# Kernel optimization log

Measured on AMD Instinct MI355X. Metric: run time of the kernel, lower is better.

The kernel has to match this reference:

```python
import jax, jax.numpy as jnp
import numpy as np

N, C, H, W = 8, 256, 64, 64
NW = 8            # n_win (regions per side)
TOPK = 4
HEADS = 16
MLP = 4 * C
SCALE = C ** -0.5  # qk_dim = dim in BiLevelRoutingAttention


def _ln(x, g, b, eps=1e-6):
    mu = x.mean(-1, keepdims=True)
    var = ((x - mu) ** 2).mean(-1, keepdims=True)
    return (x - mu) * jax.lax.rsqrt(var + eps) * g + b


def setup_inputs() -> dict:
    key = jax.random.key(0)
    ks = jax.random.split(key, 8)
    f = lambda k, shp: jax.random.normal(k, shp, jnp.float32) * 0.02
    return {
        "x": jax.random.normal(ks[0], (N, C, H, W), jnp.float32),
        "norm1_g": jnp.ones((C,), jnp.float32), "norm1_b": jnp.zeros((C,), jnp.float32),
        "qkv_w": f(ks[1], (C, 3 * C)), "qkv_b": jnp.zeros((3 * C,), jnp.float32),
        "lepe_w": f(ks[2], (5, 5, 1, C)), "lepe_b": jnp.zeros((C,), jnp.float32),
        "gamma1": -jnp.ones((C,), jnp.float32), "gamma2": -jnp.ones((C,), jnp.float32),
        "norm2_g": jnp.ones((C,), jnp.float32), "norm2_b": jnp.zeros((C,), jnp.float32),
        "mlp_w1": f(ks[3], (C, MLP)), "mlp_b1": jnp.zeros((MLP,), jnp.float32),
        "mlp_w2": f(ks[4], (MLP, C)), "mlp_b2": jnp.zeros((C,), jnp.float32),
    }


def _bra(x, qkv_w, qkv_b, lepe_w, lepe_b):
    # BiLevelRoutingAttention: x is NHWC
    n, hh, ww, c = x.shape
    h, w = hh // NW, ww // NW
    P, hw = NW * NW, h * w
    qkv = x @ qkv_w + qkv_b                    # [n,H,W,3c]
    q, k, v = qkv[..., :c], qkv[..., c:2 * c], qkv[..., 2 * c:]

    def win(t):                                 # [n,H,W,d] -> [n,P,h,w,d]
        d = t.shape[-1]
        return t.reshape(n, NW, h, NW, w, d).transpose(0, 1, 3, 2, 4, 5).reshape(n, P, h, w, d)

    qw, kw, vw = win(q), win(k), win(v)
    q_pix = qw.reshape(n, P, hw, c)
    k_pix = kw.reshape(n, P, hw, c)
    v_pix = vw.reshape(n, P, hw, c)

    # region-level routing (q/k detached; routing weights unused since mul_weight='none')
    q_win = jax.lax.stop_gradient(qw.mean((2, 3)))   # [n,P,c]
    k_win = jax.lax.stop_gradient(kw.mean((2, 3)))
    logit = jnp.einsum('npc,nqc->npq', q_win * SCALE, k_win)
    _, idx = jax.lax.top_k(logit, TOPK)              # [n,P,TOPK]

    gather = jax.vmap(lambda t, i: t[i])             # over batch
    k_sel = gather(k_pix, idx)                       # [n,P,TOPK,hw,c]
    v_sel = gather(v_pix, idx)

    dh = c // HEADS
    # channel layout is (m c): split heads on last dim
    qh = q_pix.reshape(n, P, hw, HEADS, dh).transpose(0, 1, 3, 2, 4)                       # [n,P,m,hw,dh]
    kh = k_sel.reshape(n, P, TOPK, hw, HEADS, dh).transpose(0, 1, 4, 2, 3, 5).reshape(n, P, HEADS, TOPK * hw, dh)
    vh = v_sel.reshape(n, P, TOPK, hw, HEADS, dh).transpose(0, 1, 4, 2, 3, 5).reshape(n, P, HEADS, TOPK * hw, dh)

    attn = jax.nn.softmax(jnp.einsum('npmqd,npmkd->npmqk', qh * SCALE, kh), axis=-1)
    out = jnp.einsum('npmqk,npmkd->npmqd', attn, vh)                                       # [n,P,m,hw,dh]
    out = out.transpose(0, 1, 3, 2, 4).reshape(n, P, hw, c)
    out = out.reshape(n, NW, NW, h, w, c).transpose(0, 1, 3, 2, 4, 5).reshape(n, hh, ww, c)

    # lepe: 5x5 depthwise conv over full-image v (side_dwconv=5)
    lepe = jax.lax.conv_general_dilated(
        v, lepe_w, (1, 1), 'SAME',
        dimension_numbers=('NHWC', 'HWIO', 'NHWC'),
        feature_group_count=c) + lepe_b
    return out + lepe   # wo = Identity for param_attention='qkv'


def reference(x, norm1_g, norm1_b, qkv_w, qkv_b, lepe_w, lepe_b, gamma1, gamma2,
              norm2_g, norm2_b, mlp_w1, mlp_b1, mlp_w2, mlp_b2):
    xp = x.transpose(0, 2, 3, 1)  # NCHW -> NHWC
    xp = xp + gamma1 * _bra(_ln(xp, norm1_g, norm1_b), qkv_w, qkv_b, lepe_w, lepe_b)
    z = _ln(xp, norm2_g, norm2_b)
    m = jax.nn.gelu(z @ mlp_w1 + mlp_b1, approximate=False) @ mlp_w2 + mlp_b2
    xp = xp + gamma2 * m
    return xp.transpose(0, 3, 1, 2)  # NHWC -> NCHW
```

## Files before the change

kernel.cpp:

```cpp
#include <hip/hip_runtime.h>

typedef unsigned short u16;
typedef __bf16 bf16x8 __attribute__((ext_vector_type(8)));
typedef short s16x4 __attribute__((ext_vector_type(4)));
typedef float f32x4 __attribute__((ext_vector_type(4)));

#define SCALE_ATT 0.0625f

static __device__ __forceinline__ u16 f2b(float f) {
    union { float f; unsigned u; } v; v.f = f;
    unsigned r = (v.u + 0x7fffu + ((v.u >> 16) & 1u)) >> 16;
    return (u16)r;
}
static __device__ __forceinline__ float b2f(u16 h) {
    union { unsigned u; float f; } v; v.u = ((unsigned)h) << 16;
    return v.f;
}

#if defined(__has_builtin)
#if __has_builtin(__builtin_amdgcn_mfma_f32_16x16x16bf16_1k)
#define HAVE_MFMA16 1
#endif
#if __has_builtin(__builtin_amdgcn_exp2f)
#define EXP2(x) __builtin_amdgcn_exp2f(x)
#endif
#if __has_builtin(__builtin_amdgcn_global_load_lds)
#define HAVE_GLOADLDS 1
#endif
#endif
#ifndef EXP2
#define EXP2(x) exp2f(x)
#endif

static __device__ __forceinline__ f32x4 mfma16(s16x4 a, s16x4 b, f32x4 c) {
#ifdef HAVE_MFMA16
    return __builtin_amdgcn_mfma_f32_16x16x16bf16_1k(a, b, c, 0, 0, 0);
#else
    f32x4 d;
    asm volatile("v_mfma_f32_16x16x16_bf16 %0, %1, %2, %3\n\ts_nop 7\n\ts_nop 7"
                 : "=v"(d) : "v"(a), "v"(b), "v"(c));
    return d;
#endif
}

#ifdef HAVE_GLOADLDS
static __device__ __forceinline__ void gload16(const u16* g, u16* l) {
    __builtin_amdgcn_global_load_lds(
        (const __attribute__((address_space(1))) void*)g,
        (__attribute__((address_space(3))) void*)l, 16, 0, 0);
}
#endif

__global__ void wtrans_kernel(const float* __restrict__ src, u16* __restrict__ dst,
                              int R, int C) {
    int i = blockIdx.x * 256 + threadIdx.x;
    if (i >= R * C) return;
    int r = i / C, c = i % C;
    dst[(size_t)c * R + r] = f2b(src[i]);
}

__global__ __launch_bounds__(256) void ln_xpose_kernel(
    const float* __restrict__ x, const float* __restrict__ g, const float* __restrict__ b,
    float* __restrict__ xp, u16* __restrict__ ln1, float* __restrict__ pool_part) {
    __shared__ float xs[256][65];
    __shared__ float ps[4][64], ps2[4][64];
    __shared__ float mvmu[64], mvrs[64];
    int nb = blockIdx.x; int n = nb >> 6, y = nb & 63;
    int t = threadIdx.x;
    const float4* src = (const float4*)(x + ((size_t)(n * 256 + t) * 64 + y) * 64);
    for (int x4 = 0; x4 < 16; ++x4) {
        float4 v = src[x4];
        xs[t][x4 * 4 + 0] = v.x; xs[t][x4 * 4 + 1] = v.y;
        xs[t][x4 * 4 + 2] = v.z; xs[t][x4 * 4 + 3] = v.w;
    }
    __syncthreads();
    int part = t >> 6, l = t & 63;
    float s1 = 0.f, s2 = 0.f;
    for (int c = 0; c < 64; ++c) { float v = xs[part * 64 + c][l]; s1 += v; s2 += v * v; }
    ps[part][l] = s1; ps2[part][l] = s2;
    __syncthreads();
    if (t < 64) {
        float su = ps[0][t] + ps[1][t] + ps[2][t] + ps[3][t];
        float sq = ps2[0][t] + ps2[1][t] + ps2[2][t] + ps2[3][t];
        float mu = su * (1.f / 256.f);
        float var = sq * (1.f / 256.f) - mu * mu;
        mvmu[t] = mu; mvrs[t] = rsqrtf(var + 1e-6f);
    }
    __syncthreads();
    float gc = g[t], bc = b[t];
    size_t tokbase = (size_t)nb * 64;
    float pw = 0.f;
    for (int xx = 0; xx < 64; ++xx) {
        float raw = xs[t][xx];
        float val = (raw - mvmu[xx]) * mvrs[xx] * gc + bc;
        size_t tok = tokbase + xx;
        xp[tok * 256 + t] = raw;
        ln1[tok * 256 + t] = f2b(val);
        pw += val;
        if ((xx & 7) == 7) {
            pool_part[((size_t)nb * 8 + (xx >> 3)) * 256 + t] = pw;
            pw = 0.f;
        }
    }
}

__global__ void pool_reduce_kernel(const float* __restrict__ pool_part,
                                   float* __restrict__ pooled) {
    int nb = blockIdx.x; int n = nb >> 6, p = nb & 63;
    int wi = p >> 3, wj = p & 7;
    int t = threadIdx.x;
    float s = 0.f;
    for (int r = 0; r < 8; ++r)
        s += pool_part[((size_t)((n * 64 + wi * 8 + r) * 8 + wj)) * 256 + t];
    pooled[(size_t)nb * 256 + t] = s * (1.f / 64.f);
}

__global__ void qkwin_kernel(const float* __restrict__ pooled,
                             const float* __restrict__ qkv_w, const float* __restrict__ qkv_b,
                             float* __restrict__ qk_win) {
    __shared__ float pr[256];
    int nb = blockIdx.x; int t = threadIdx.x;
    pr[t] = pooled[(size_t)nb * 256 + t];
    __syncthreads();
    float aq = qkv_b[t], ak = qkv_b[256 + t];
    for (int k = 0; k < 256; ++k) {
        float pv = pr[k];
        aq += pv * qkv_w[(size_t)k * 768 + t];
        ak += pv * qkv_w[(size_t)k * 768 + 256 + t];
    }
    qk_win[(size_t)nb * 512 + t] = aq;
    qk_win[(size_t)nb * 512 + 256 + t] = ak;
}

__global__ void routing_kernel(const float* __restrict__ qk_win, int* __restrict__ idxp) {
    __shared__ float lg_[64];
    int nb = blockIdx.x; int n = nb >> 6;
    int t = threadIdx.x;
    const float* qw = qk_win + (size_t)nb * 512;
    const float* kw = qk_win + (size_t)(n * 64 + t) * 512 + 256;
    float s = 0.f;
    for (int c = 0; c < 256; ++c) s += qw[c] * kw[c];
    lg_[t] = s * SCALE_ATT;
    __syncthreads();
    if (t == 0) {
        for (int j = 0; j < 4; ++j) {
            float best = -INFINITY; int bi = 0;
            for (int q = 0; q < 64; ++q) if (lg_[q] > best) { best = lg_[q]; bi = q; }
            idxp[nb * 4 + j] = bi;
            lg_[bi] = -INFINITY;
        }
    }
}

template <int EPI>
__global__ __launch_bounds__(256) void gemm_kernel(
    const u16* __restrict__ A, const u16* __restrict__ Bt,
    const float* __restrict__ bias, u16* __restrict__ outb,
    int M, int Nn, int K,
    const float* __restrict__ resid_in, const float* __restrict__ gamma,
    float* __restrict__ resid_out) {
    __shared__ u16 As[4096];
    __shared__ u16 Bs[4096];
    int t = threadIdx.x;
    int rowBase = blockIdx.x * 128, colBase = blockIdx.y * 128;
    int wid = t >> 6, lane = t & 63;
    int wr = (wid >> 1) * 64, wc = (wid & 1) * 64;
    int lr = lane & 15, g = lane >> 4;
    f32x4 acc[4][4] = {};

    int rA0 = wid * 32 + (lane >> 2);
    int rA1 = rA0 + 16;
    int cs0 = (lane & 3) ^ ((rA0 >> 1) & 3);
    int cs1 = (lane & 3) ^ ((rA1 >> 1) & 3);
    const u16* gA0 = A + (size_t)(rowBase + rA0) * K + cs0 * 8;
    const u16* gA1 = A + (size_t)(rowBase + rA1) * K + cs1 * 8;
    const u16* gB0 = Bt + (size_t)(colBase + rA0) * K + cs0 * 8;
    const u16* gB1 = Bt + (size_t)(colBase + rA1) * K + cs1 * 8;
    u16* lA0 = &As[(wid * 2 + 0) * 512];
    u16* lA1 = &As[(wid * 2 + 1) * 512];
    u16* lB0 = &Bs[(wid * 2 + 0) * 512];
    u16* lB1 = &Bs[(wid * 2 + 1) * 512];

    int cSwz = (g * 16) ^ (((lr >> 1) & 3) << 4);
    const char* pA = (const char*)As;
    const char* pB = (const char*)Bs;

    for (int k0 = 0; k0 < K; k0 += 32) {
#ifdef HAVE_GLOADLDS
        gload16(gA0 + k0, lA0);
        gload16(gA1 + k0, lA1);
        gload16(gB0 + k0, lB0);
        gload16(gB1 + k0, lB1);
        __syncthreads();
#else
        float4 a0 = *(const float4*)(gA0 + k0);
        float4 a1 = *(const float4*)(gA1 + k0);
        float4 b0 = *(const float4*)(gB0 + k0);
        float4 b1 = *(const float4*)(gB1 + k0);
        __syncthreads();
        *(float4*)&lA0[lane * 8] = a0;
        *(float4*)&lA1[lane * 8] = a1;
        *(float4*)&lB0[lane * 8] = b0;
        *(float4*)&lB1[lane * 8] = b1;
        __syncthreads();
#endif
        bf16x8 af[4], bfr[4];
        #pragma unroll
        for (int m = 0; m < 4; ++m)
            af[m] = *(const bf16x8*)(pA + (wr + m * 16 + lr) * 64 + cSwz);
        #pragma unroll
        for (int nn = 0; nn < 4; ++nn)
            bfr[nn] = *(const bf16x8*)(pB + (wc + nn * 16 + lr) * 64 + cSwz);
        #pragma unroll
        for (int m = 0; m < 4; ++m)
            #pragma unroll
            for (int nn = 0; nn < 4; ++nn)
                acc[m][nn] = __builtin_amdgcn_mfma_f32_16x16x32_bf16(af[m], bfr[nn], acc[m][nn], 0, 0, 0);
        __syncthreads();
    }
    #pragma unroll
    for (int m = 0; m < 4; ++m)
        #pragma unroll
        for (int nn = 0; nn < 4; ++nn) {
            int col = colBase + wc + nn * 16 + lr;
            float bcol = bias[col];
            #pragma unroll
            for (int r = 0; r < 4; ++r) {
                int row = rowBase + wr + m * 16 + g * 4 + r;
                float v = acc[m][nn][r] + bcol;
                if constexpr (EPI == 0) {
                    outb[(size_t)row * Nn + col] = f2b(v);
                } else if constexpr (EPI == 1) {
                    float gl = 0.5f * v * (1.f + erff(v * 0.70710678118654752f));
                    outb[(size_t)row * Nn + col] = f2b(gl);
                } else {
                    float yv = resid_in[(size_t)row * 256 + col] + gamma[col] * v;
                    resid_out[(size_t)row * 256 + col] = yv;
                }
            }
        }
}

__global__ __launch_bounds__(256) void lepe_kernel(
    const u16* __restrict__ qkv, const float* __restrict__ w,
    const float* __restrict__ bias, u16* __restrict__ lepe) {
    __shared__ u16 vt[5][64][64];
    int nb = blockIdx.x, cg = blockIdx.y;
    int n = nb >> 6, y = nb & 63;
    int t = threadIdx.x;
    {
        int xs = t >> 3, cs = t & 7;
        #pragma unroll
        for (int r = 0; r < 5; ++r) {
            int yy = y - 2 + r;
            bool ok = (yy >= 0 && yy <= 63);
            #pragma unroll
            for (int half = 0; half < 2; ++half) {
                int x = xs + half * 32;
                float4 v = {0.f, 0.f, 0.f, 0.f};
                if (ok)
                    v = *(const float4*)(qkv +
                        ((size_t)((n * 64 + yy) * 64 + x)) * 768 + 512 + cg * 64 + cs * 8);
                *(float4*)&vt[r][x][cs * 8] = v;
            }
        }
    }
    __syncthreads();
    int c = t & 63, x0 = (t >> 6) * 16;
    float wv[25];
    #pragma unroll
    for (int i = 0; i < 25; ++i) wv[i] = w[i * 256 + cg * 64 + c];
    float bc = bias[cg * 64 + c];
    float win[5][5];
    #pragma unroll
    for (int r = 0; r < 5; ++r)
        #pragma unroll
        for (int j = 0; j < 4; ++j) {
            int x2 = x0 - 2 + j;
            win[r][j] = (x2 >= 0) ? b2f(vt[r][x2][c]) : 0.f;
        }
    #pragma unroll
    for (int xi = 0; xi < 16; ++xi) {
        int xx = x0 + xi;
        int xl = xx + 2;
        #pragma unroll
        for (int r = 0; r < 5; ++r)
            win[r][4] = (xl <= 63) ? b2f(vt[r][xl][c]) : 0.f;
        float s = bc;
        #pragma unroll
        for (int r = 0; r < 5; ++r)
            #pragma unroll
            for (int j = 0; j < 5; ++j)
                s = fmaf(wv[r * 5 + j], win[r][j], s);
        lepe[((size_t)nb * 64 + xx) * 256 + cg * 64 + c] = f2b(s);
        #pragma unroll
        for (int r = 0; r < 5; ++r)
            #pragma unroll
            for (int j = 0; j < 4; ++j)
                win[r][j] = win[r][j + 1];
    }
}

__global__ __launch_bounds__(512) void attn_kernel(
    const u16* __restrict__ qkv, const int* __restrict__ idxp,
    float* __restrict__ attn_out) {
    __shared__ __align__(16) char smem_[39424];
    u16 (*qs)[36]   = (u16 (*)[36])smem_;
    u16 (*ks)[36]   = (u16 (*)[36])(smem_ + 4608);
    u16 (*vts)[256] = (u16 (*)[256])(smem_ + 23040);
    float (*os)[36] = (float (*)[36])(smem_ + 4608);
    int nb = blockIdx.x, hg = blockIdx.y;
    int n = nb >> 6, p = nb & 63;
    int y0 = (p >> 3) * 8, x0 = (p & 7) * 8;
    int t = threadIdx.x;
    int w0 = idxp[nb * 4 + 0], w1 = idxp[nb * 4 + 1];
    int w2 = idxp[nb * 4 + 2], w3 = idxp[nb * 4 + 3];
    {
        int tok = t >> 3, seg = t & 7;
        int tokg = (n * 64 + y0 + (tok >> 3)) * 64 + x0 + (tok & 7);
        *(uint2*)&qs[tok][seg * 4] =
            *(const uint2*)(qkv + (size_t)tokg * 768 + hg * 32 + seg * 4);
    }
    {
        int key = t & 255, half = t >> 8;
        int ws = (key >> 6) == 0 ? w0 : (key >> 6) == 1 ? w1 : (key >> 6) == 2 ? w2 : w3;
        int kp = key & 63;
        int tokk = (n * 64 + (ws >> 3) * 8 + (kp >> 3)) * 64 + (ws & 7) * 8 + (kp & 7);
        const u16* kbase = qkv + (size_t)tokk * 768 + 256 + hg * 32 + half * 16;
        *(uint2*)&ks[key][half * 16 + 0]  = *(const uint2*)(kbase + 0);
        *(uint2*)&ks[key][half * 16 + 4]  = *(const uint2*)(kbase + 4);
        *(uint2*)&ks[key][half * 16 + 8]  = *(const uint2*)(kbase + 8);
        *(uint2*)&ks[key][half * 16 + 12] = *(const uint2*)(kbase + 12);
        const u16* vbase = kbase + 256;
        union { float4 f[2]; u16 u[16]; } vu;
        vu.f[0] = *(const float4*)vbase;
        vu.f[1] = *(const float4*)(vbase + 8);
        #pragma unroll
        for (int c2 = 0; c2 < 16; ++c2)
            vts[half * 16 + c2][key ^ (c2 << 2)] = vu.u[c2];
    }
    __syncthreads();

    int wid = t >> 6, lane = t & 63, lr = lane & 15, g = lane >> 4;
    int hh = wid & 1, q0 = (wid >> 1) * 16, c0 = hh * 16;
    f32x4 zf4 = {0.f, 0.f, 0.f, 0.f};
    s16x4 qf = *(const s16x4*)&qs[q0 + lr][c0 + g * 4];
    f32x4 sacc[16];
    __builtin_amdgcn_s_setprio(1);
    #pragma unroll
    for (int kt = 0; kt < 16; ++kt) {
        s16x4 kf = *(const s16x4*)&ks[kt * 16 + lr][c0 + g * 4];
        sacc[kt] = mfma16(kf, qf, zf4);
    }
    __builtin_amdgcn_s_setprio(0);
    float mx = fmaxf(fmaxf(sacc[0][0], sacc[0][1]), fmaxf(sacc[0][2], sacc[0][3]));
    #pragma unroll
    for (int kt = 1; kt < 16; ++kt) {
        mx = fmaxf(mx, fmaxf(sacc[kt][0], sacc[kt][1]));
        mx = fmaxf(mx, fmaxf(sacc[kt][2], sacc[kt][3]));
    }
    mx = fmaxf(mx, __shfl_xor(mx, 16, 64));
    mx = fmaxf(mx, __shfl_xor(mx, 32, 64));
    const float k1 = 0.09016844005556021f;
    float negmk = -mx * k1;
    float dsum = 0.f;
    s16x4 pf[16];
    #pragma unroll
    for (int kt = 0; kt < 16; ++kt) {
        float e0 = EXP2(fmaf(sacc[kt][0], k1, negmk));
        float e1 = EXP2(fmaf(sacc[kt][1], k1, negmk));
        float e2 = EXP2(fmaf(sacc[kt][2], k1, negmk));
        float e3 = EXP2(fmaf(sacc[kt][3], k1, negmk));
        dsum += (e0 + e1) + (e2 + e3);
        union { unsigned u[2]; s16x4 s; } pk;
        asm("v_cvt_pk_bf16_f32 %0, %1, %2" : "=v"(pk.u[0]) : "v"(e0), "v"(e1));
        asm("v_cvt_pk_bf16_f32 %0, %1, %2" : "=v"(pk.u[1]) : "v"(e2), "v"(e3));
        pf[kt] = pk.s;
    }
    dsum += __shfl_xor(dsum, 16, 64);
    dsum += __shfl_xor(dsum, 32, 64);
    float rden = 1.f / dsum;
    __syncthreads();
    f32x4 o0 = zf4, o1 = zf4;
    __builtin_amdgcn_s_setprio(1);
    #pragma unroll
    for (int kt = 0; kt < 16; kt += 2) {
        s16x4 v0 = *(const s16x4*)&vts[c0 + lr][(kt * 16 + g * 4) ^ (lr << 2)];
        o0 = mfma16(v0, pf[kt], o0);
        s16x4 v1 = *(const s16x4*)&vts[c0 + lr][((kt + 1) * 16 + g * 4) ^ (lr << 2)];
        o1 = mfma16(v1, pf[kt + 1], o1);
    }
    __builtin_amdgcn_s_setprio(0);
    #pragma unroll
    for (int r = 0; r < 4; ++r)
        os[q0 + lr][c0 + g * 4 + r] = (o0[r] + o1[r]) * rden;
    __syncthreads();
    {
        int tok = t >> 3, cs = (t & 7) * 4;
        int tokg = (n * 64 + y0 + (tok >> 3)) * 64 + x0 + (tok & 7);
        *(float4*)(attn_out + (size_t)tokg * 256 + hg * 32 + cs) =
            *(const float4*)&os[tok][cs];
    }
}

__global__ __launch_bounds__(256) void resid1_ln2_kernel(
    const float* __restrict__ xp, const float* __restrict__ attn,
    const u16* __restrict__ lepe, const float* __restrict__ g1,
    const float* __restrict__ n2g, const float* __restrict__ n2b,
    float* __restrict__ xp1, u16* __restrict__ z) {
    __shared__ float w1s[4], w2s[4];
    size_t tok = blockIdx.x;
    int t = threadIdx.x;
    float x1 = xp[tok * 256 + t] + g1[t] * (attn[tok * 256 + t] + b2f(lepe[tok * 256 + t]));
    xp1[tok * 256 + t] = x1;
    float s1 = x1, s2 = x1 * x1;
    for (int off = 1; off < 64; off <<= 1) {
        s1 += __shfl_xor(s1, off, 64);
        s2 += __shfl_xor(s2, off, 64);
    }
    int wid = t >> 6;
    if ((t & 63) == 0) { w1s[wid] = s1; w2s[wid] = s2; }
    __syncthreads();
    s1 = w1s[0] + w1s[1] + w1s[2] + w1s[3];
    s2 = w2s[0] + w2s[1] + w2s[2] + w2s[3];
    float mu = s1 * (1.f / 256.f);
    float var = s2 * (1.f / 256.f) - mu * mu;
    float rs = rsqrtf(var + 1e-6f);
    z[tok * 256 + t] = f2b((x1 - mu) * rs * n2g[t] + n2b[t]);
}

__global__ __launch_bounds__(256) void out_xpose_kernel(
    const float* __restrict__ yout, float* __restrict__ outp) {
    __shared__ float ys[256][65];
    int nb = blockIdx.x; int n = nb >> 6, y = nb & 63;
    int t = threadIdx.x;
    for (int xx = 0; xx < 64; ++xx)
        ys[t][xx] = yout[((size_t)nb * 64 + xx) * 256 + t];
    __syncthreads();
    float4* dst = (float4*)(outp + ((size_t)(n * 256 + t) * 64 + y) * 64);
    for (int x4 = 0; x4 < 16; ++x4) {
        float4 v = { ys[t][x4 * 4 + 0], ys[t][x4 * 4 + 1],
                     ys[t][x4 * 4 + 2], ys[t][x4 * 4 + 3] };
        dst[x4] = v;
    }
}

extern "C" void kernel_launch(void* const* d_in, const int* in_sizes, int n_in,
                              void* d_out, int out_size, void* d_ws, size_t ws_size,
                              hipStream_t stream) {
    (void)in_sizes; (void)n_in; (void)out_size; (void)ws_size;
    const float* x      = (const float*)d_in[0];
    const float* n1g    = (const float*)d_in[1];
    const float* n1b    = (const float*)d_in[2];
    const float* qkv_w  = (const float*)d_in[3];
    const float* qkv_b  = (const float*)d_in[4];
    const float* lepe_w = (const float*)d_in[5];
    const float* lepe_b = (const float*)d_in[6];
    const float* g1     = (const float*)d_in[7];
    const float* g2     = (const float*)d_in[8];
    const float* n2g    = (const float*)d_in[9];
    const float* n2b    = (const float*)d_in[10];
    const float* w1     = (const float*)d_in[11];
    const float* b1     = (const float*)d_in[12];
    const float* w2     = (const float*)d_in[13];
    const float* b2     = (const float*)d_in[14];
    float* outp = (float*)d_out;
    char* ws = (char*)d_ws;

    float* xp        = (float*)(ws + 0);
    u16*   ln1       = (u16*)(ws + 33554432);
    u16*   qkv       = (u16*)(ws + 50331648);
    float* attn_out  = (float*)(ws + 100663296);
    u16*   lepe      = (u16*)(ws + 134217728);
    u16*   zbuf      = (u16*)(ws + 150994944);
    float* pool_part = (float*)(ws + 167772160);
    float* pooled    = (float*)(ws + 171966464);
    float* qk_win    = (float*)(ws + 172490752);
    int*   idxb      = (int*)(ws + 173539328);
    u16*   wt_qkv    = (u16*)(ws + 173547520);
    u16*   wt_m1     = (u16*)(ws + 173940736);
    u16*   wt_m2     = (u16*)(ws + 174465024);
    u16*   hbuf      = ln1;
    float* xp1       = outp;
    float* yout      = attn_out;

    wtrans_kernel<<<768, 256, 0, stream>>>(qkv_w, wt_qkv, 256, 768);
    wtrans_kernel<<<1024, 256, 0, stream>>>(w1, wt_m1, 256, 1024);
    wtrans_kernel<<<1024, 256, 0, stream>>>(w2, wt_m2, 1024, 256);

    ln_xpose_kernel<<<512, 256, 0, stream>>>(x, n1g, n1b, xp, ln1, pool_part);
    pool_reduce_kernel<<<512, 256, 0, stream>>>(pool_part, pooled);
    qkwin_kernel<<<512, 256, 0, stream>>>(pooled, qkv_w, qkv_b, qk_win);
    routing_kernel<<<512, 64, 0, stream>>>(qk_win, idxb);

    gemm_kernel<0><<<dim3(256, 6), 256, 0, stream>>>(
        ln1, wt_qkv, qkv_b, qkv, 32768, 768, 256, nullptr, nullptr, nullptr);

    lepe_kernel<<<dim3(512, 4), 256, 0, stream>>>(qkv, lepe_w, lepe_b, lepe);
    attn_kernel<<<dim3(512, 8), 512, 0, stream>>>(qkv, idxb, attn_out);

    resid1_ln2_kernel<<<32768, 256, 0, stream>>>(xp, attn_out, lepe, g1, n2g, n2b, xp1, zbuf);

    gemm_kernel<1><<<dim3(256, 8), 256, 0, stream>>>(
        zbuf, wt_m1, b1, hbuf, 32768, 1024, 256, nullptr, nullptr, nullptr);
    gemm_kernel<2><<<dim3(256, 2), 256, 0, stream>>>(
        hbuf, wt_m2, b2, nullptr, 32768, 256, 1024, xp1, g2, yout);

    out_xpose_kernel<<<512, 256, 0, stream>>>(yout, outp);
}
```

Measured before the change: 278.4 us.

## Use tanh-approx GELU, bf16 attention output, and native bf16 conversion

```diff
diff --git a/kernel.cpp b/kernel.cpp
--- a/kernel.cpp
+++ b/kernel.cpp
@@ -8,9 +8,9 @@
 #define SCALE_ATT 0.0625f
 
 static __device__ __forceinline__ u16 f2b(float f) {
-    union { float f; unsigned u; } v; v.f = f;
-    unsigned r = (v.u + 0x7fffu + ((v.u >> 16) & 1u)) >> 16;
-    return (u16)r;
+    __bf16 h = (__bf16)f;
+    union { __bf16 b; u16 u; } v; v.b = h;
+    return v.u;
 }
 static __device__ __forceinline__ float b2f(u16 h) {
     union { unsigned u; float f; } v; v.u = ((unsigned)h) << 16;
@@ -24,12 +24,18 @@
 #if __has_builtin(__builtin_amdgcn_exp2f)
 #define EXP2(x) __builtin_amdgcn_exp2f(x)
 #endif
+#if __has_builtin(__builtin_amdgcn_rcpf)
+#define RCP(x) __builtin_amdgcn_rcpf(x)
+#endif
 #if __has_builtin(__builtin_amdgcn_global_load_lds)
 #define HAVE_GLOADLDS 1
 #endif
 #endif
 #ifndef EXP2
 #define EXP2(x) exp2f(x)
+#endif
+#ifndef RCP
+#define RCP(x) (1.0f / (x))
 #endif
 
 static __device__ __forceinline__ f32x4 mfma16(s16x4 a, s16x4 b, f32x4 c) {
@@ -50,6 +56,15 @@
         (__attribute__((address_space(3))) void*)l, 16, 0, 0);
 }
 #endif
+
+static __device__ __forceinline__ float gelu_fast(float v) {
+    float v2 = v * v;
+    float w = fmaf(v2, 0.044715f, 1.0f);
+    float arg = v * w * 2.30211754f;
+    float e = EXP2(arg);
+    float r = RCP(e + 1.0f);
+    return fmaf(-v, r, v);
+}
 
 __global__ void wtrans_kernel(const float* __restrict__ src, u16* __restrict__ dst,
                               int R, int C) {
@@ -231,8 +246,7 @@
                 if constexpr (EPI == 0) {
                     outb[(size_t)row * Nn + col] = f2b(v);
                 } else if constexpr (EPI == 1) {
-                    float gl = 0.5f * v * (1.f + erff(v * 0.70710678118654752f));
-                    outb[(size_t)row * Nn + col] = f2b(gl);
+                    outb[(size_t)row * Nn + col] = f2b(gelu_fast(v));
                 } else {
                     float yv = resid_in[(size_t)row * 256 + col] + gamma[col] * v;
                     resid_out[(size_t)row * 256 + col] = yv;
@@ -303,7 +317,7 @@
 
 __global__ __launch_bounds__(512) void attn_kernel(
     const u16* __restrict__ qkv, const int* __restrict__ idxp,
-    float* __restrict__ attn_out) {
+    u16* __restrict__ attn_out) {
     __shared__ __align__(16) char smem_[39424];
     u16 (*qs)[36]   = (u16 (*)[36])smem_;
     u16 (*ks)[36]   = (u16 (*)[36])(smem_ + 4608);
@@ -398,20 +412,24 @@
     {
         int tok = t >> 3, cs = (t & 7) * 4;
         int tokg = (n * 64 + y0 + (tok >> 3)) * 64 + x0 + (tok & 7);
-        *(float4*)(attn_out + (size_t)tokg * 256 + hg * 32 + cs) =
-            *(const float4*)&os[tok][cs];
+        float f0 = os[tok][cs + 0], f1 = os[tok][cs + 1];
+        float f2 = os[tok][cs + 2], f3 = os[tok][cs + 3];
+        uint2 pk;
+        asm("v_cvt_pk_bf16_f32 %0, %1, %2" : "=v"(pk.x) : "v"(f0), "v"(f1));
+        asm("v_cvt_pk_bf16_f32 %0, %1, %2" : "=v"(pk.y) : "v"(f2), "v"(f3));
+        *(uint2*)(attn_out + (size_t)tokg * 256 + hg * 32 + cs) = pk;
     }
 }
 
 __global__ __launch_bounds__(256) void resid1_ln2_kernel(
-    const float* __restrict__ xp, const float* __restrict__ attn,
+    const float* __restrict__ xp, const u16* __restrict__ attn,
     const u16* __restrict__ lepe, const float* __restrict__ g1,
     const float* __restrict__ n2g, const float* __restrict__ n2b,
     float* __restrict__ xp1, u16* __restrict__ z) {
     __shared__ float w1s[4], w2s[4];
     size_t tok = blockIdx.x;
     int t = threadIdx.x;
-    float x1 = xp[tok * 256 + t] + g1[t] * (attn[tok * 256 + t] + b2f(lepe[tok * 256 + t]));
+    float x1 = xp[tok * 256 + t] + g1[t] * (b2f(attn[tok * 256 + t]) + b2f(lepe[tok * 256 + t]));
     xp1[tok * 256 + t] = x1;
     float s1 = x1, s2 = x1 * x1;
     for (int off = 1; off < 64; off <<= 1) {
@@ -470,7 +488,7 @@
     float* xp        = (float*)(ws + 0);
     u16*   ln1       = (u16*)(ws + 33554432);
     u16*   qkv       = (u16*)(ws + 50331648);
-    float* attn_out  = (float*)(ws + 100663296);
+    u16*   attn_b    = (u16*)(ws + 100663296);
     u16*   lepe      = (u16*)(ws + 134217728);
     u16*   zbuf      = (u16*)(ws + 150994944);
     float* pool_part = (float*)(ws + 167772160);
@@ -482,7 +500,7 @@
     u16*   wt_m2     = (u16*)(ws + 174465024);
     u16*   hbuf      = ln1;
     float* xp1       = outp;
-    float* yout      = attn_out;
+    float* yout      = (float*)(ws + 100663296);
 
     wtrans_kernel<<<768, 256, 0, stream>>>(qkv_w, wt_qkv, 256, 768);
     wtrans_kernel<<<1024, 256, 0, stream>>>(w1, wt_m1, 256, 1024);
@@ -497,9 +515,9 @@
         ln1, wt_qkv, qkv_b, qkv, 32768, 768, 256, nullptr, nullptr, nullptr);
 
     lepe_kernel<<<dim3(512, 4), 256, 0, stream>>>(qkv, lepe_w, lepe_b, lepe);
-    attn_kernel<<<dim3(512, 8), 512, 0, stream>>>(qkv, idxb, attn_out);
-
-    resid1_ln2_kernel<<<32768, 256, 0, stream>>>(xp, attn_out, lepe, g1, n2g, n2b, xp1, zbuf);
+    attn_kernel<<<dim3(512, 8), 512, 0, stream>>>(qkv, idxb, attn_b);
+
+    resid1_ln2_kernel<<<32768, 256, 0, stream>>>(xp, attn_b, lepe, g1, n2g, n2b, xp1, zbuf);
 
     gemm_kernel<1><<<dim3(256, 8), 256, 0, stream>>>(
         zbuf, wt_m1, b1, hbuf, 32768, 1024, 256, nullptr, nullptr, nullptr);
```

Result: faster. 270.5 us (-2.9%).
